# Kernel optimization log

Hardware: AMD Instinct MI355X
Metric: run time of the kernel (lower is better)

Reference implementation:

```python
import jax, jax.numpy as jnp
import numpy as np

G = 16  # grid (window) size, fixed in the module


def _ln_channels(x, w, b, eps=1e-5):
    # LayerNorm4D: normalize over channel dim of NCHW
    mu = x.mean(axis=1, keepdims=True)
    var = ((x - mu) ** 2).mean(axis=1, keepdims=True)
    return (x - mu) / jnp.sqrt(var + eps) * w[None, :, None, None] + b[None, :, None, None]


def setup_inputs() -> dict:
    key = jax.random.key(0)
    ks = jax.random.split(key, 8)
    B, C, H, W = 8, 256, 128, 128
    C8, F = C // 8, 4 * C
    s = 0.02
    return {
        "x": jax.random.normal(ks[0], (B, C, H, W), jnp.float32),
        "Wq": jax.random.normal(ks[1], (C8, C), jnp.float32) * s,
        "Wk": jax.random.normal(ks[2], (C8, C), jnp.float32) * s,
        "Wv": jax.random.normal(ks[3], (C, C), jnp.float32) * s,
        "gamma": jnp.float32(1.0),
        "W1": jax.random.normal(ks[4], (F, C), jnp.float32) * s,
        "b1": jnp.zeros((F,), jnp.float32),
        "W2": jax.random.normal(ks[5], (C, F), jnp.float32) * s,
        "b2": jnp.zeros((C,), jnp.float32),
        "ln1_w": jnp.ones((C,), jnp.float32),
        "ln1_b": jnp.zeros((C,), jnp.float32),
        "ln2_w": jnp.ones((C,), jnp.float32),
        "ln2_b": jnp.zeros((C,), jnp.float32),
    }


def reference(x, Wq, Wk, Wv, gamma, W1, b1, W2, b2, ln1_w, ln1_b, ln2_w, ln2_b):
    B, C, H, W = x.shape
    nh, nw = H // G, W // G
    N = G * G  # tokens per window
    # gather all 16x16 windows into the batch dim: [B*nh*nw, C, N]
    xw = x.reshape(B, C, nh, G, nw, G).transpose(0, 2, 4, 1, 3, 5).reshape(B * nh * nw, C, N)
    # SAGAN-style self-attention within each window
    q = jnp.einsum('oc,bcn->bno', Wq, xw)                 # [Bw, N, C/8]
    k = jnp.einsum('oc,bcn->bon', Wk, xw)                 # [Bw, C/8, N]
    attn = jax.nn.softmax(jnp.einsum('bno,bom->bnm', q, k), axis=-1)  # [Bw, N, N]
    v = jnp.einsum('oc,bcn->bon', Wv, xw)                 # [Bw, C, N]
    out = jnp.einsum('bcn,bmn->bcm', v, attn)             # v @ attn^T
    aw = gamma * out + xw
    # scatter windows back to NCHW
    xa = aw.reshape(B, nh, nw, C, G, G).transpose(0, 3, 1, 4, 2, 5).reshape(B, C, H, W)
    # FFN: 1x1 conv -> GELU(exact) -> 1x1 conv (dropout is identity in eval)
    h1 = jax.nn.gelu(jnp.einsum('fc,bchw->bfhw', W1, xa) + b1[None, :, None, None], approximate=False)
    y = jnp.einsum('cf,bfhw->bchw', W2, h1) + b2[None, :, None, None]
    x2 = xa + _ln_channels(y, ln1_w, ln1_b)
    return x2 + _ln_channels(x2, ln2_w, ln2_b)
```

## Files before the change

### kernel.cpp

```cpp
#include <hip/hip_runtime.h>
#include <hip/hip_bf16.h>

#define C_DIM 256
#define HW_DIM 16384
#define F_DIM 1024

typedef __hip_bfloat16 bf16;
typedef short short8 __attribute__((ext_vector_type(8)));
typedef float f32x4 __attribute__((ext_vector_type(4)));

__device__ __forceinline__ float bf2f(unsigned short u) {
  unsigned int x = ((unsigned int)u) << 16;
  return __uint_as_float(x);
}
__device__ __forceinline__ unsigned short f2bfbits(float v) {
  bf16 h = __float2bfloat16(v);
  return *(unsigned short*)&h;
}

__global__ __launch_bounds__(256) void prep_weights(
    const float* __restrict__ Wq, const float* __restrict__ Wk,
    const float* __restrict__ Wv, const float* __restrict__ W1,
    const float* __restrict__ W2, unsigned short* __restrict__ Wqkv,
    unsigned short* __restrict__ W1s, unsigned short* __restrict__ W2s) {
  int i = blockIdx.x * 256 + threadIdx.x;
  if (i < 320 * 256) {
    int r = i >> 8, c = i & 255;
    float v;
    if (r < 32)      v = Wq[r * 256 + c];
    else if (r < 64) v = Wk[(r - 32) * 256 + c];
    else             v = Wv[(r - 64) * 256 + c];
    Wqkv[i] = f2bfbits(v);
  }
  if (i < 32768) {
    int ft = i >> 9, ks = (i >> 6) & 7, l = i & 63;
    int f = ft * 16 + (l & 15), kb = ks * 32 + (l >> 4) * 8;
    #pragma unroll
    for (int j = 0; j < 8; ++j)
      W1s[i * 8 + j] = f2bfbits(W1[f * 256 + kb + j]);
  }
  if (i < 32768) {
    int ct = i >> 11, gks = (i >> 6) & 31, l = i & 63;
    int c = ct * 16 + (l & 15), fb = gks * 32 + (l >> 4) * 8;
    #pragma unroll
    for (int j = 0; j < 8; ++j)
      W2s[i * 8 + j] = f2bfbits(W2[c * 1024 + fb + j]);
  }
}

__global__ __launch_bounds__(256) void qkvproj_kernel(
    const float* __restrict__ x, const unsigned short* __restrict__ Wqkv,
    unsigned short* __restrict__ Qw, unsigned short* __restrict__ Kw,
    unsigned short* __restrict__ Vw) {
  __shared__ __align__(16) short Xs[256][68];
  const int bid = blockIdx.x;
  const int win = bid >> 2, mc = bid & 3;
  const int b = win >> 6, wh = (win >> 3) & 7, ww = win & 7;
  const int m0 = mc * 64;
  const int tid = threadIdx.x;
  const int wv = tid >> 6, l = tid & 63;
  const int t = l & 15, q = l >> 4;

  #pragma unroll
  for (int rep = 0; rep < 4; ++rep) {
    int seg = rep * 256 + tid;
    int c = seg >> 2, gh_l = seg & 3;
    const float* xp = x + (((size_t)(b * 256 + c) * 128) + wh * 16 + mc * 4 + gh_l) * 128 + ww * 16;
    #pragma unroll
    for (int s = 0; s < 4; ++s) {
      float4 v = *(const float4*)(xp + s * 4);
      ushort4 u;
      u.x = f2bfbits(v.x); u.y = f2bfbits(v.y);
      u.z = f2bfbits(v.z); u.w = f2bfbits(v.w);
      *(ushort4*)&Xs[c][gh_l * 16 + s * 4] = u;
    }
  }
  __syncthreads();

  for (int mt = 0; mt < 4; ++mt) {
    short8 Bf[8];
    #pragma unroll
    for (int ks = 0; ks < 8; ++ks) {
      short8 bb;
      #pragma unroll
      for (int j = 0; j < 8; ++j)
        bb[j] = Xs[ks * 32 + q * 8 + j][mt * 16 + t];
      Bf[ks] = bb;
    }
    #pragma unroll
    for (int rti = 0; rti < 5; ++rti) {
      const int rt = wv * 5 + rti;
      const int r0 = rt * 16;
      f32x4 acc = (f32x4){0.f, 0.f, 0.f, 0.f};
      #pragma unroll
      for (int ks = 0; ks < 8; ++ks) {
        short8 av = *(const short8*)(Wqkv + (size_t)(r0 + t) * 256 + ks * 32 + q * 8);
        acc = __builtin_amdgcn_mfma_f32_16x16x32_bf16(av, Bf[ks], acc, 0, 0, 0);
      }
      const int n = m0 + mt * 16 + t;
      if (rt < 4) {
        ushort4 u;
        u.x = f2bfbits(acc[0]); u.y = f2bfbits(acc[1]);
        u.z = f2bfbits(acc[2]); u.w = f2bfbits(acc[3]);
        unsigned short* dst = (rt < 2) ? Qw : Kw;
        int o0 = (rt & 1) * 16 + q * 4;
        *(ushort4*)(dst + ((size_t)win * 256 + n) * 32 + o0) = u;
      } else {
        #pragma unroll
        for (int r = 0; r < 4; ++r) {
          int c = r0 - 64 + q * 4 + r;
          Vw[((size_t)win * 256 + c) * 256 + n] = f2bfbits(acc[r]);
        }
      }
    }
  }
}

__global__ __launch_bounds__(1024) void attn_fused_kernel(
    const unsigned short* __restrict__ Qw, const unsigned short* __restrict__ Kw,
    const unsigned short* __restrict__ Vw, const float* __restrict__ x,
    const float* __restrict__ gamma, unsigned short* __restrict__ XAw) {
  __shared__ __align__(16) short Ps[256][72];
  __shared__ float Lpart[4][4][64];
  __shared__ float Ls[256];

  const int win = blockIdx.x;
  const int b = win >> 6, wh = (win >> 3) & 7, ww = win & 7;
  const int tid = threadIdx.x;
  const int wid = tid >> 6, l = tid & 63;
  const int t = l & 15, q = l >> 4;
  const int wr = wid >> 2, wc = wid & 3;

  f32x4 Oacc[4][4];
  #pragma unroll
  for (int k = 0; k < 4; ++k)
    #pragma unroll
    for (int i = 0; i < 4; ++i)
      Oacc[k][i] = (f32x4){0.f, 0.f, 0.f, 0.f};
  float lsum[16];
  #pragma unroll
  for (int e = 0; e < 16; ++e) lsum[e] = 0.f;

  const unsigned short* Qb = Qw + (size_t)win * 256 * 32;
  const unsigned short* Kb = Kw + (size_t)win * 256 * 32;
  const unsigned short* Vb = Vw + (size_t)win * 65536;

  short8 aq[4];
  #pragma unroll
  for (int i = 0; i < 4; ++i)
    aq[i] = *(const short8*)(Qb + (size_t)((wr * 4 + i) * 16 + t) * 32 + q * 8);

  for (int mcc = 0; mcc < 4; ++mcc) {
    {
      const int m0s = (mcc * 4 + wc) * 16;
      short8 bk = *(const short8*)(Kb + (size_t)(m0s + t) * 32 + q * 8);
      f32x4 sv[4];
      #pragma unroll
      for (int i = 0; i < 4; ++i)
        sv[i] = __builtin_amdgcn_mfma_f32_16x16x32_bf16(aq[i], bk, (f32x4){0.f,0.f,0.f,0.f}, 0, 0, 0);
      #pragma unroll
      for (int i = 0; i < 4; ++i) {
        #pragma unroll
        for (int r = 0; r < 4; ++r) {
          float e = __expf(sv[i][r]);
          lsum[i * 4 + r] += e;
          Ps[(wr * 4 + i) * 16 + q * 4 + r][wc * 16 + t] = (short)f2bfbits(e);
        }
      }
    }
    __syncthreads();
    #pragma unroll
    for (int ks2 = 0; ks2 < 2; ++ks2) {
      short8 ap[4], bv[4];
      #pragma unroll
      for (int i = 0; i < 4; ++i)
        ap[i] = *(const short8*)&Ps[(wr * 4 + i) * 16 + t][ks2 * 32 + q * 8];
      #pragma unroll
      for (int k = 0; k < 4; ++k)
        bv[k] = *(const short8*)(Vb + (size_t)((wc * 4 + k) * 16 + t) * 256 + mcc * 64 + ks2 * 32 + q * 8);
      #pragma unroll
      for (int k = 0; k < 4; ++k)
        #pragma unroll
        for (int i = 0; i < 4; ++i)
          Oacc[k][i] = __builtin_amdgcn_mfma_f32_16x16x32_bf16(bv[k], ap[i], Oacc[k][i], 0, 0, 0);
    }
    __syncthreads();
  }

  #pragma unroll
  for (int mask = 1; mask < 16; mask <<= 1)
    #pragma unroll
    for (int e = 0; e < 16; ++e)
      lsum[e] += __shfl_xor(lsum[e], mask);
  if (t == 0) {
    #pragma unroll
    for (int i = 0; i < 4; ++i)
      *(float4*)&Lpart[wr][wc][i * 16 + q * 4] =
          make_float4(lsum[i * 4 + 0], lsum[i * 4 + 1], lsum[i * 4 + 2], lsum[i * 4 + 3]);
  }
  __syncthreads();
  if (tid < 256) {
    int wrr = tid >> 6, nl = tid & 63;
    float s = Lpart[wrr][0][nl] + Lpart[wrr][1][nl] + Lpart[wrr][2][nl] + Lpart[wrr][3][nl];
    Ls[tid] = gamma[0] / s;
  }
  __syncthreads();

  const float* xb = x + (size_t)b * 256 * 16384 + ((size_t)(wh * 16 + wr * 4)) * 128 + ww * 16 + t;
  #pragma unroll
  for (int i = 0; i < 4; ++i) {
    const int n = (wr * 4 + i) * 16 + t;
    const float ls = Ls[n];
    unsigned short* dst = XAw + ((size_t)win * 256 + n) * 256;
    #pragma unroll
    for (int k = 0; k < 4; ++k) {
      const int cb = (wc * 4 + k) * 16 + q * 4;
      ushort4 u;
      unsigned short* up = (unsigned short*)&u;
      #pragma unroll
      for (int r = 0; r < 4; ++r) {
        float xa = xb[(size_t)(cb + r) * 16384 + i * 128];
        float o = ls * Oacc[k][i][r] + xa;
        up[r] = f2bfbits(o);
      }
      *(ushort4*)(dst + cb) = u;
    }
  }
}

__global__ __launch_bounds__(256, 3) void ffn_mfma_kernel(
    const unsigned short* __restrict__ XAw,
    const unsigned short* __restrict__ W1s, const unsigned short* __restrict__ W2s,
    const float* __restrict__ b1, const float* __restrict__ b2,
    const float* __restrict__ ln1w, const float* __restrict__ ln1b,
    const float* __restrict__ ln2w, const float* __restrict__ ln2b,
    float* __restrict__ out) {
  __shared__ __align__(16) short Xt[64][264];
  __shared__ __align__(16) short Ht[64][136];
  __shared__ float red[2][4][64];

  const int bid = blockIdx.x;
  const int win = bid >> 2, mc = bid & 3;
  const int b = win >> 6, wh = (win >> 3) & 7, ww = win & 7;
  const int tid = threadIdx.x;
  const int wv = tid >> 6, l = tid & 63;
  const int p = l & 15, q = l >> 4;
  const unsigned short* XWb = XAw + ((size_t)win * 256 + mc * 64) * 256;

  #pragma unroll
  for (int rep = 0; rep < 8; ++rep) {
    int s = rep * 256 + tid;
    int row = s >> 5, col8 = (s & 31) * 8;
    short8 v = *(const short8*)(XWb + (size_t)row * 256 + col8);
    *(short8*)&Xt[row][col8] = v;
  }
  __syncthreads();

  f32x4 Yacc[4][4];
  #pragma unroll
  for (int i = 0; i < 4; ++i)
    #pragma unroll
    for (int pt = 0; pt < 4; ++pt)
      Yacc[i][pt] = (f32x4){0.f, 0.f, 0.f, 0.f};

  const short8* W1s8 = (const short8*)W1s;
  const short8* W2s8 = (const short8*)W2s;

  for (int fc = 0; fc < 8; ++fc) {
    f32x4 Hacc[2][4];
    #pragma unroll
    for (int i = 0; i < 2; ++i)
      #pragma unroll
      for (int pt = 0; pt < 4; ++pt)
        Hacc[i][pt] = (f32x4){0.f, 0.f, 0.f, 0.f};
    const int f0 = (fc * 8 + wv * 2) * 8;
    #pragma unroll
    for (int ks = 0; ks < 8; ++ks) {
      short8 a0 = W1s8[(f0 + ks) * 64 + l];
      short8 a1 = W1s8[(f0 + 8 + ks) * 64 + l];
      #pragma unroll
      for (int pt = 0; pt < 4; ++pt) {
        short8 bf = *(const short8*)&Xt[pt * 16 + p][ks * 32 + q * 8];
        Hacc[0][pt] = __builtin_amdgcn_mfma_f32_16x16x32_bf16(a0, bf, Hacc[0][pt], 0, 0, 0);
        Hacc[1][pt] = __builtin_amdgcn_mfma_f32_16x16x32_bf16(a1, bf, Hacc[1][pt], 0, 0, 0);
      }
    }
    __syncthreads();
    #pragma unroll
    for (int i = 0; i < 2; ++i) {
      float4 bv1 = *(const float4*)(b1 + fc * 128 + wv * 32 + i * 16 + q * 4);
      #pragma unroll
      for (int pt = 0; pt < 4; ++pt) {
        ushort4 hbv;
        unsigned short* hp = (unsigned short*)&hbv;
        #pragma unroll
        for (int r = 0; r < 4; ++r) {
          float v = Hacc[i][pt][r] + ((const float*)&bv1)[r];
          float u = 0.7978845608f * fmaf(0.044715f * v, v * v, v);
          float e = __expf(2.f * u);
          float g = v - v / (e + 1.f);
          hp[r] = f2bfbits(g);
        }
        *(ushort4*)&Ht[pt * 16 + p][wv * 32 + i * 16 + q * 4] = hbv;
      }
    }
    __syncthreads();
    #pragma unroll
    for (int fs = 0; fs < 4; ++fs) {
      short8 av[4];
      #pragma unroll
      for (int i = 0; i < 4; ++i)
        av[i] = W2s8[((wv * 4 + i) * 32 + fc * 4 + fs) * 64 + l];
      #pragma unroll
      for (int pt = 0; pt < 4; ++pt) {
        short8 bf = *(const short8*)&Ht[pt * 16 + p][fs * 32 + q * 8];
        #pragma unroll
        for (int i = 0; i < 4; ++i)
          Yacc[i][pt] = __builtin_amdgcn_mfma_f32_16x16x32_bf16(av[i], bf, Yacc[i][pt], 0, 0, 0);
      }
    }
  }

  #pragma unroll
  for (int i = 0; i < 4; ++i) {
    float4 bb = *(const float4*)(b2 + wv * 64 + i * 16 + q * 4);
    #pragma unroll
    for (int pt = 0; pt < 4; ++pt)
      #pragma unroll
      for (int r = 0; r < 4; ++r)
        Yacc[i][pt][r] += ((const float*)&bb)[r];
  }

  #pragma unroll
  for (int pt = 0; pt < 4; ++pt) {
    float ss = 0.f, sq = 0.f;
    #pragma unroll
    for (int i = 0; i < 4; ++i)
      #pragma unroll
      for (int r = 0; r < 4; ++r) { float v = Yacc[i][pt][r]; ss += v; sq += v * v; }
    ss += __shfl_xor(ss, 16); sq += __shfl_xor(sq, 16);
    ss += __shfl_xor(ss, 32); sq += __shfl_xor(sq, 32);
    if (l < 16) { red[0][wv][pt * 16 + l] = ss; red[1][wv][pt * 16 + l] = sq; }
  }
  __syncthreads();
  if (tid < 64) {
    float S  = red[0][0][tid] + red[0][1][tid] + red[0][2][tid] + red[0][3][tid];
    float Q2 = red[1][0][tid] + red[1][1][tid] + red[1][2][tid] + red[1][3][tid];
    float m = S * 0.00390625f;
    float va = Q2 * 0.00390625f - m * m;
    red[0][0][tid] = m; red[1][0][tid] = rsqrtf(va + 1e-5f);
  }
  __syncthreads();
  #pragma unroll
  for (int i = 0; i < 4; ++i) {
    float4 w1v = *(const float4*)(ln1w + wv * 64 + i * 16 + q * 4);
    float4 b1v = *(const float4*)(ln1b + wv * 64 + i * 16 + q * 4);
    #pragma unroll
    for (int pt = 0; pt < 4; ++pt) {
      int px = pt * 16 + p;
      float mu = red[0][0][px], rs = red[1][0][px];
      #pragma unroll
      for (int r = 0; r < 4; ++r) {
        int c = wv * 64 + i * 16 + q * 4 + r;
        float xa = bf2f((unsigned short)Xt[px][c]);
        Yacc[i][pt][r] = xa + (Yacc[i][pt][r] - mu) * rs * ((const float*)&w1v)[r] + ((const float*)&b1v)[r];
      }
    }
  }
  __syncthreads();
  #pragma unroll
  for (int pt = 0; pt < 4; ++pt) {
    float ss = 0.f, sq = 0.f;
    #pragma unroll
    for (int i = 0; i < 4; ++i)
      #pragma unroll
      for (int r = 0; r < 4; ++r) { float v = Yacc[i][pt][r]; ss += v; sq += v * v; }
    ss += __shfl_xor(ss, 16); sq += __shfl_xor(sq, 16);
    ss += __shfl_xor(ss, 32); sq += __shfl_xor(sq, 32);
    if (l < 16) { red[0][wv][pt * 16 + l] = ss; red[1][wv][pt * 16 + l] = sq; }
  }
  __syncthreads();
  if (tid < 64) {
    float S  = red[0][0][tid] + red[0][1][tid] + red[0][2][tid] + red[0][3][tid];
    float Q2 = red[1][0][tid] + red[1][1][tid] + red[1][2][tid] + red[1][3][tid];
    float m = S * 0.00390625f;
    float va = Q2 * 0.00390625f - m * m;
    red[0][0][tid] = m; red[1][0][tid] = rsqrtf(va + 1e-5f);
  }
  __syncthreads();
  #pragma unroll
  for (int i = 0; i < 4; ++i) {
    float4 w2v = *(const float4*)(ln2w + wv * 64 + i * 16 + q * 4);
    float4 b2v = *(const float4*)(ln2b + wv * 64 + i * 16 + q * 4);
    #pragma unroll
    for (int pt = 0; pt < 4; ++pt) {
      int px = pt * 16 + p;
      float mu = red[0][0][px], rs = red[1][0][px];
      #pragma unroll
      for (int r = 0; r < 4; ++r) {
        int c = wv * 64 + i * 16 + q * 4 + r;
        float x2 = Yacc[i][pt][r];
        float o = x2 + (x2 - mu) * rs * ((const float*)&w2v)[r] + ((const float*)&b2v)[r];
        out[(((size_t)(b * 256 + c) * 128) + wh * 16 + mc * 4 + pt) * 128 + ww * 16 + p] = o;
      }
    }
  }
}

extern "C" void kernel_launch(void* const* d_in, const int* in_sizes, int n_in,
                              void* d_out, int out_size, void* d_ws, size_t ws_size,
                              hipStream_t stream) {
  const float* x     = (const float*)d_in[0];
  const float* Wq    = (const float*)d_in[1];
  const float* Wk    = (const float*)d_in[2];
  const float* Wv    = (const float*)d_in[3];
  const float* gamma = (const float*)d_in[4];
  const float* W1    = (const float*)d_in[5];
  const float* b1    = (const float*)d_in[6];
  const float* W2    = (const float*)d_in[7];
  const float* b2    = (const float*)d_in[8];
  const float* ln1w  = (const float*)d_in[9];
  const float* ln1b  = (const float*)d_in[10];
  const float* ln2w  = (const float*)d_in[11];
  const float* ln2b  = (const float*)d_in[12];
  float* out = (float*)d_out;

  char* wsb = (char*)d_ws;
  unsigned short* XAw  = (unsigned short*)wsb;
  unsigned short* Vw   = (unsigned short*)(wsb + 67108864);
  unsigned short* Qw   = (unsigned short*)(wsb + 134217728);
  unsigned short* Kw   = (unsigned short*)(wsb + 142606336);
  unsigned short* Wqkv = (unsigned short*)(wsb + 150994944);
  unsigned short* W1s  = (unsigned short*)(wsb + 151158784);
  unsigned short* W2s  = (unsigned short*)(wsb + 151683072);

  prep_weights<<<1024, 256, 0, stream>>>(Wq, Wk, Wv, W1, W2, Wqkv, W1s, W2s);
  qkvproj_kernel<<<2048, 256, 0, stream>>>(x, Wqkv, Qw, Kw, Vw);
  attn_fused_kernel<<<512, 1024, 0, stream>>>(Qw, Kw, Vw, x, gamma, XAw);
  ffn_mfma_kernel<<<2048, 256, 0, stream>>>(XAw, W1s, W2s, b1, b2, ln1w, ln1b, ln2w, ln2b, out);
}
```

Measured before the change: 686.2 us.

## Pre-swizzle input into MFMA fragment layout and drop LDS staging

Adds an xprep kernel that converts x to bf16 once and stores it in MFMA B-fragment order per window. The QKV projection, attention residual and FFN kernels then read fragments straight from global memory, with no LDS transpose or staging. Removing the Xt buffer frees shared memory, and the FFN launch bound goes from 3 to 4 blocks per CU. The cost is an extra kernel launch plus a 64MB bf16 intermediate. The residual x in the attention output is now the bf16-rounded value rather than the fp32 input.

```diff
diff --git a/kernel.cpp b/kernel.cpp
--- a/kernel.cpp
+++ b/kernel.cpp
@@ -17,6 +17,7 @@
   bf16 h = __float2bfloat16(v);
   return *(unsigned short*)&h;
 }
+
 
 __global__ __launch_bounds__(256) void prep_weights(
     const float* __restrict__ Wq, const float* __restrict__ Wk,
@@ -48,45 +49,41 @@
   }
 }
 
+__global__ __launch_bounds__(256) void xprep_kernel(
+    const float* __restrict__ x, unsigned short* __restrict__ Xfrag) {
+  const int gtid = blockIdx.x * 256 + threadIdx.x;
+  const int win = gtid >> 13;
+  const int rem = gtid & 8191;
+  const int mt = rem >> 9, ks = (rem >> 6) & 7, l = rem & 63;
+  const int t = l & 15, q = l >> 4;
+  const int b = win >> 6, wh = (win >> 3) & 7, ww = win & 7;
+  const int h = wh * 16 + mt, w = ww * 16 + t;
+  const int c0 = ks * 32 + q * 8;
+  const float* xp = x + ((size_t)(b * 256 + c0) * 128 + h) * 128 + w;
+  short8 v;
+  #pragma unroll
+  for (int j = 0; j < 8; ++j)
+    v[j] = (short)f2bfbits(xp[(size_t)j * 16384]);
+  *(short8*)(Xfrag + (size_t)gtid * 8) = v;
+}
+
 __global__ __launch_bounds__(256) void qkvproj_kernel(
-    const float* __restrict__ x, const unsigned short* __restrict__ Wqkv,
+    const unsigned short* __restrict__ Xfrag, const unsigned short* __restrict__ Wqkv,
     unsigned short* __restrict__ Qw, unsigned short* __restrict__ Kw,
     unsigned short* __restrict__ Vw) {
-  __shared__ __align__(16) short Xs[256][68];
   const int bid = blockIdx.x;
   const int win = bid >> 2, mc = bid & 3;
-  const int b = win >> 6, wh = (win >> 3) & 7, ww = win & 7;
   const int m0 = mc * 64;
   const int tid = threadIdx.x;
   const int wv = tid >> 6, l = tid & 63;
   const int t = l & 15, q = l >> 4;
-
-  #pragma unroll
-  for (int rep = 0; rep < 4; ++rep) {
-    int seg = rep * 256 + tid;
-    int c = seg >> 2, gh_l = seg & 3;
-    const float* xp = x + (((size_t)(b * 256 + c) * 128) + wh * 16 + mc * 4 + gh_l) * 128 + ww * 16;
-    #pragma unroll
-    for (int s = 0; s < 4; ++s) {
-      float4 v = *(const float4*)(xp + s * 4);
-      ushort4 u;
-      u.x = f2bfbits(v.x); u.y = f2bfbits(v.y);
-      u.z = f2bfbits(v.z); u.w = f2bfbits(v.w);
-      *(ushort4*)&Xs[c][gh_l * 16 + s * 4] = u;
-    }
-  }
-  __syncthreads();
+  const unsigned short* Xb = Xfrag + (size_t)win * 65536;
 
   for (int mt = 0; mt < 4; ++mt) {
     short8 Bf[8];
     #pragma unroll
-    for (int ks = 0; ks < 8; ++ks) {
-      short8 bb;
-      #pragma unroll
-      for (int j = 0; j < 8; ++j)
-        bb[j] = Xs[ks * 32 + q * 8 + j][mt * 16 + t];
-      Bf[ks] = bb;
-    }
+    for (int ks = 0; ks < 8; ++ks)
+      Bf[ks] = *(const short8*)(Xb + (((size_t)(mc * 4 + mt) * 8 + ks) * 64 + l) * 8);
     #pragma unroll
     for (int rti = 0; rti < 5; ++rti) {
       const int rt = wv * 5 + rti;
@@ -118,14 +115,13 @@
 
 __global__ __launch_bounds__(1024) void attn_fused_kernel(
     const unsigned short* __restrict__ Qw, const unsigned short* __restrict__ Kw,
-    const unsigned short* __restrict__ Vw, const float* __restrict__ x,
-    const float* __restrict__ gamma, unsigned short* __restrict__ XAw) {
+    const unsigned short* __restrict__ Vw, const unsigned short* __restrict__ Xfrag,
+    const float* __restrict__ gamma, unsigned short* __restrict__ XAfrag) {
   __shared__ __align__(16) short Ps[256][72];
   __shared__ float Lpart[4][4][64];
   __shared__ float Ls[256];
 
   const int win = blockIdx.x;
-  const int b = win >> 6, wh = (win >> 3) & 7, ww = win & 7;
   const int tid = threadIdx.x;
   const int wid = tid >> 6, l = tid & 63;
   const int t = l & 15, q = l >> 4;
@@ -206,36 +202,35 @@
   }
   __syncthreads();
 
-  const float* xb = x + (size_t)b * 256 * 16384 + ((size_t)(wh * 16 + wr * 4)) * 128 + ww * 16 + t;
+  const unsigned short* Xres = Xfrag + (size_t)win * 65536;
+  unsigned short* XAb = XAfrag + (size_t)win * 65536;
   #pragma unroll
   for (int i = 0; i < 4; ++i) {
     const int n = (wr * 4 + i) * 16 + t;
     const float ls = Ls[n];
-    unsigned short* dst = XAw + ((size_t)win * 256 + n) * 256;
     #pragma unroll
     for (int k = 0; k < 4; ++k) {
-      const int cb = (wc * 4 + k) * 16 + q * 4;
+      const size_t off = (((size_t)(wr * 4 + i) * 8 + wc * 2 + (k >> 1)) * 64 +
+                          ((k & 1) * 2 + (q >> 1)) * 16 + t) * 8 + (q & 1) * 4;
+      ushort4 xa4 = *(const ushort4*)(Xres + off);
+      const unsigned short* xp = (const unsigned short*)&xa4;
       ushort4 u;
       unsigned short* up = (unsigned short*)&u;
       #pragma unroll
-      for (int r = 0; r < 4; ++r) {
-        float xa = xb[(size_t)(cb + r) * 16384 + i * 128];
-        float o = ls * Oacc[k][i][r] + xa;
-        up[r] = f2bfbits(o);
-      }
-      *(ushort4*)(dst + cb) = u;
-    }
-  }
-}
-
-__global__ __launch_bounds__(256, 3) void ffn_mfma_kernel(
-    const unsigned short* __restrict__ XAw,
+      for (int r = 0; r < 4; ++r)
+        up[r] = f2bfbits(ls * Oacc[k][i][r] + bf2f(xp[r]));
+      *(ushort4*)(XAb + off) = u;
+    }
+  }
+}
+
+__global__ __launch_bounds__(256, 4) void ffn_mfma_kernel(
+    const unsigned short* __restrict__ XAfrag,
     const unsigned short* __restrict__ W1s, const unsigned short* __restrict__ W2s,
     const float* __restrict__ b1, const float* __restrict__ b2,
     const float* __restrict__ ln1w, const float* __restrict__ ln1b,
     const float* __restrict__ ln2w, const float* __restrict__ ln2b,
     float* __restrict__ out) {
-  __shared__ __align__(16) short Xt[64][264];
   __shared__ __align__(16) short Ht[64][136];
   __shared__ float red[2][4][64];
 
@@ -245,16 +240,7 @@
   const int tid = threadIdx.x;
   const int wv = tid >> 6, l = tid & 63;
   const int p = l & 15, q = l >> 4;
-  const unsigned short* XWb = XAw + ((size_t)win * 256 + mc * 64) * 256;
-
-  #pragma unroll
-  for (int rep = 0; rep < 8; ++rep) {
-    int s = rep * 256 + tid;
-    int row = s >> 5, col8 = (s & 31) * 8;
-    short8 v = *(const short8*)(XWb + (size_t)row * 256 + col8);
-    *(short8*)&Xt[row][col8] = v;
-  }
-  __syncthreads();
+  const unsigned short* XAb = XAfrag + (size_t)win * 65536;
 
   f32x4 Yacc[4][4];
   #pragma unroll
@@ -280,7 +266,7 @@
       short8 a1 = W1s8[(f0 + 8 + ks) * 64 + l];
       #pragma unroll
       for (int pt = 0; pt < 4; ++pt) {
-        short8 bf = *(const short8*)&Xt[pt * 16 + p][ks * 32 + q * 8];
+        short8 bf = *(const short8*)(XAb + (((size_t)(mc * 4 + pt) * 8 + ks) * 64 + l) * 8);
         Hacc[0][pt] = __builtin_amdgcn_mfma_f32_16x16x32_bf16(a0, bf, Hacc[0][pt], 0, 0, 0);
         Hacc[1][pt] = __builtin_amdgcn_mfma_f32_16x16x32_bf16(a1, bf, Hacc[1][pt], 0, 0, 0);
       }
@@ -359,12 +345,13 @@
     for (int pt = 0; pt < 4; ++pt) {
       int px = pt * 16 + p;
       float mu = red[0][0][px], rs = red[1][0][px];
-      #pragma unroll
-      for (int r = 0; r < 4; ++r) {
-        int c = wv * 64 + i * 16 + q * 4 + r;
-        float xa = bf2f((unsigned short)Xt[px][c]);
-        Yacc[i][pt][r] = xa + (Yacc[i][pt][r] - mu) * rs * ((const float*)&w1v)[r] + ((const float*)&b1v)[r];
-      }
+      const size_t off = (((size_t)(mc * 4 + pt) * 8 + wv * 2 + (i >> 1)) * 64 +
+                          ((i & 1) * 2 + (q >> 1)) * 16 + p) * 8 + (q & 1) * 4;
+      ushort4 xa4 = *(const ushort4*)(XAb + off);
+      const unsigned short* xp = (const unsigned short*)&xa4;
+      #pragma unroll
+      for (int r = 0; r < 4; ++r)
+        Yacc[i][pt][r] = bf2f(xp[r]) + (Yacc[i][pt][r] - mu) * rs * ((const float*)&w1v)[r] + ((const float*)&b1v)[r];
     }
   }
   __syncthreads();
@@ -426,16 +413,18 @@
   float* out = (float*)d_out;
 
   char* wsb = (char*)d_ws;
-  unsigned short* XAw  = (unsigned short*)wsb;
-  unsigned short* Vw   = (unsigned short*)(wsb + 67108864);
-  unsigned short* Qw   = (unsigned short*)(wsb + 134217728);
-  unsigned short* Kw   = (unsigned short*)(wsb + 142606336);
-  unsigned short* Wqkv = (unsigned short*)(wsb + 150994944);
-  unsigned short* W1s  = (unsigned short*)(wsb + 151158784);
-  unsigned short* W2s  = (unsigned short*)(wsb + 151683072);
+  unsigned short* XAfrag = (unsigned short*)wsb;
+  unsigned short* Vw     = (unsigned short*)(wsb + 67108864);
+  unsigned short* Xfrag  = (unsigned short*)(wsb + 134217728);
+  unsigned short* Qw     = (unsigned short*)(wsb + 201326592);
+  unsigned short* Kw     = (unsigned short*)(wsb + 209715200);
+  unsigned short* Wqkv   = (unsigned short*)(wsb + 218103808);
+  unsigned short* W1s    = (unsigned short*)(wsb + 218267648);
+  unsigned short* W2s    = (unsigned short*)(wsb + 218791936);
 
   prep_weights<<<1024, 256, 0, stream>>>(Wq, Wk, Wv, W1, W2, Wqkv, W1s, W2s);
-  qkvproj_kernel<<<2048, 256, 0, stream>>>(x, Wqkv, Qw, Kw, Vw);
-  attn_fused_kernel<<<512, 1024, 0, stream>>>(Qw, Kw, Vw, x, gamma, XAw);
-  ffn_mfma_kernel<<<2048, 256, 0, stream>>>(XAw, W1s, W2s, b1, b2, ln1w, ln1b, ln2w, ln2b, out);
-}
+  xprep_kernel<<<16384, 256, 0, stream>>>(x, Xfrag);
+  qkvproj_kernel<<<2048, 256, 0, stream>>>(Xfrag, Wqkv, Qw, Kw, Vw);
+  attn_fused_kernel<<<512, 1024, 0, stream>>>(Qw, Kw, Vw, Xfrag, gamma, XAfrag);
+  ffn_mfma_kernel<<<2048, 256, 0, stream>>>(XAfrag, W1s, W2s, b1, b2, ln1w, ln1b, ln2w, ln2b, out);
+}
```

New measurement: 1.013 ms. 47.6% more time.
